# Optimization experiments

Measured on AMD Instinct MI355X. Metric: run time of the kernel, lower is better.

## Reference

```python
import jax, jax.numpy as jnp
import numpy as np

B, T, N, D = 2048, 24, 231, 512
EPS = 1e-5


def _conv(x, W, b):
    # NCHW conv, stride 2, VALID padding (Conv2d k=3, s=2, p=0)
    y = jax.lax.conv_general_dilated(x, W, (2, 2), 'VALID',
                                     dimension_numbers=('NCHW', 'OIHW', 'NCHW'))
    return y + b[None, :, None, None]


def _bn(x, g, b, m, v):
    # inference-mode BatchNorm2d
    inv = jax.lax.rsqrt(v + EPS)
    return (x - m[None, :, None, None]) * (inv * g)[None, :, None, None] + b[None, :, None, None]


def _proj(x, W1, b1, g1, be1, m1, v1, W2, b2, g2, be2, m2, v2):
    y = _bn(jax.nn.relu(_conv(x, W1, b1)), g1, be1, m1, v1)   # [B,32,5,10]
    y = _bn(jax.nn.relu(_conv(y, W2, b2)), g2, be2, m2, v2)   # [B,16,2,4]
    return y


def setup_inputs() -> dict:
    key = jax.random.key(0)
    ks = jax.random.split(key, 16)

    def rn(k, shape, s=1.0):
        return jax.random.normal(k, shape, jnp.float32) * s

    inp = {
        'data0': rn(ks[0], (B, T, N, 2)),
        'data2': rn(ks[1], (B, T, N, 2)),
        'cache': rn(ks[2], (B, 4, 4, N, 4)),
        'timesnet_cache': rn(ks[3], (B, 4, 4, D)),
        'bike_start': rn(ks[4], (B, 4, N)),
        'bike_end': rn(ks[5], (B, 4, N)),
        'taxi_start': rn(ks[6], (B, 4, N)),
        'taxi_end': rn(ks[7], (B, 4, N)),
        'intermediate_output': rn(ks[8], (B, T, D)),
    }
    # conv + batchnorm params for query_proj ('q') and key_proj ('k')
    for pre, i in (('q', 9), ('k', 12)):
        inp[pre + 'W1'] = rn(ks[i], (32, 16, 3, 3), 0.08)
        inp[pre + 'b1'] = jnp.zeros((32,), jnp.float32)
        inp[pre + 'g1'] = jnp.ones((32,), jnp.float32)
        inp[pre + 'be1'] = jnp.zeros((32,), jnp.float32)
        inp[pre + 'm1'] = jnp.zeros((32,), jnp.float32)
        inp[pre + 'v1'] = jnp.ones((32,), jnp.float32)
        inp[pre + 'W2'] = rn(ks[i + 1], (16, 32, 3, 3), 0.06)
        inp[pre + 'b2'] = jnp.zeros((16,), jnp.float32)
        inp[pre + 'g2'] = jnp.ones((16,), jnp.float32)
        inp[pre + 'be2'] = jnp.zeros((16,), jnp.float32)
        inp[pre + 'm2'] = jnp.zeros((16,), jnp.float32)
        inp[pre + 'v2'] = jnp.ones((16,), jnp.float32)
    return inp


def reference(data0, data2, cache, timesnet_cache,
              bike_start, bike_end, taxi_start, taxi_end, intermediate_output,
              qW1, qb1, qg1, qbe1, qm1, qv1, qW2, qb2, qg2, qbe2, qm2, qv2,
              kW1, kb1, kg1, kbe1, km1, kv1, kW2, kb2, kg2, kbe2, km2, kv2):
    # --- cache plumbing (pred_model outputs supplied directly) ---
    new_predict = jnp.stack([bike_start, bike_end, taxi_start, taxi_end], axis=-1)  # [B,4,N,4]
    updated_cache = jnp.concatenate([new_predict[:, None], cache[:, -3:]], axis=1)  # [B,4,4,N,4]
    results = updated_cache[:, :, 0]                                                # [B,4,N,4]
    new_timesnet_cache = jnp.concatenate(
        [intermediate_output[:, -4:, :][:, None], timesnet_cache[:, -3:]], axis=1)  # [B,4,4,D]

    # --- build q, k: [B,16,231] ---
    q = jnp.concatenate([data0[:, -4:], data2[:, -4:]], axis=-1)     # [B,4,N,4]
    q = q.transpose(0, 1, 3, 2).reshape(B, 16, N)
    k = results.transpose(0, 1, 3, 2).reshape(B, 16, N)

    # --- MultiTensorAttention ---
    Q = _proj(q.reshape(B, 16, 11, 21), qW1, qb1, qg1, qbe1, qm1, qv1,
              qW2, qb2, qg2, qbe2, qm2, qv2).reshape(B, 16, -1)       # [B,16,8]
    K = _proj(k.reshape(B, 16, 11, 21), kW1, kb1, kg1, kbe1, km1, kv1,
              kW2, kb2, kg2, kbe2, km2, kv2).reshape(B, 16, -1)       # [B,16,8]
    d_k = Q.shape[-1]
    scores = jnp.einsum('bid,bjd->bij', Q, K) / jnp.sqrt(jnp.float32(d_k))  # [B,16,16]

    # extract the 4 diagonal 4x4 blocks (equivalent to unfold/unfold + stack)
    s = scores.reshape(B, 4, 4, 4, 4)                # [B, blk_i, in_i, blk_j, in_j]
    idx = jnp.arange(4)
    diag = jnp.moveaxis(s[:, idx, :, idx, :], 0, 1)  # [B,4,4,4]
    attn = jax.nn.softmax(diag, axis=-1)
    weights = jnp.mean(attn, axis=2)                 # [B,4,4]

    return (weights, updated_cache, new_predict, new_timesnet_cache)
```

## Files before the change

### kernel.cpp

```cpp
#include <hip/hip_runtime.h>
#include <math.h>


struct ProjParams {
  const float *W1, *b1, *g1, *be1, *m1, *v1;
  const float *W2, *b2, *g2, *be2, *m2, *v2;
};

__global__ __launch_bounds__(256) void proj_kernel(
    const float* __restrict__ data0, const float* __restrict__ data2,
    const float* __restrict__ cache,
    const float* __restrict__ bike_start, const float* __restrict__ bike_end,
    const float* __restrict__ taxi_start, const float* __restrict__ taxi_end,
    ProjParams qp, ProjParams kp,
    float* __restrict__ qbuf, float* __restrict__ kbuf)
{
  const int b   = blockIdx.y;
  const int p   = blockIdx.x;
  const int tid = threadIdx.x;

  __shared__ float xs[16 * 231];
  __shared__ float w1s[144 * 32];
  __shared__ float w2s[288 * 16];
  __shared__ float y1s[32 * 50];
  __shared__ float sc1[32], sh1[32], sc2[16], sh2[16];

  const ProjParams P = p ? kp : qp;

  if (p == 0) {
    for (int e = tid; e < 16 * 231; e += 256) {
      int ic = e / 231, n = e - ic * 231;
      int t = ic >> 2, f = ic & 3;
      const float* src = (f < 2) ? data0 : data2;
      xs[e] = src[((b * 24 + 20 + t) * 231 + n) * 2 + (f & 1)];
    }
  } else {
    for (int e = tid; e < 16 * 231; e += 256) {
      int ic = e / 231, n = e - ic * 231;
      int s = ic >> 2, f = ic & 3;
      float v;
      if (s == 0) {
        const float* src = (f == 0) ? bike_start : (f == 1) ? bike_end
                         : (f == 2) ? taxi_start : taxi_end;
        v = src[b * 924 + n];
      } else {
        v = cache[((b * 4 + s) * 924 + n) * 4 + f];
      }
      xs[e] = v;
    }
  }
  for (int e = tid; e < 4608; e += 256) {
    int oc = e / 144, rem = e - oc * 144;
    w1s[rem * 32 + oc] = P.W1[e];
  }
  for (int e = tid; e < 4608; e += 256) {
    int oc = e / 288, rem = e - oc * 288;
    w2s[rem * 16 + oc] = P.W2[e];
  }
  if (tid < 32) {
    float s = rsqrtf(P.v1[tid] + 1e-5f) * P.g1[tid];
    sc1[tid] = s;
    sh1[tid] = P.be1[tid] - P.m1[tid] * s;
  } else if (tid < 48) {
    int oc = tid - 32;
    float s = rsqrtf(P.v2[oc] + 1e-5f) * P.g2[oc];
    sc2[oc] = s;
    sh2[oc] = P.be2[oc] - P.m2[oc] * s;
  }
  __syncthreads();

  if (tid < 80) {
    const int ocg = tid / 10, r = tid - ocg * 10;
    const int oh = r >> 1, owg = r & 1;
    const int oc0 = ocg * 4, ow0 = owg * 5;
    float acc[4][5];
#pragma unroll
    for (int i = 0; i < 4; ++i) {
      float bi = P.b1[oc0 + i];
#pragma unroll
      for (int j = 0; j < 5; ++j) acc[i][j] = bi;
    }
    for (int ic = 0; ic < 16; ++ic) {
      const float* xrow = &xs[ic * 231 + 2 * oh * 21 + 2 * ow0];
      const float* wrow = &w1s[ic * 9 * 32 + oc0];
#pragma unroll
      for (int kh = 0; kh < 3; ++kh) {
#pragma unroll
        for (int kw = 0; kw < 3; ++kw) {
          const float4 wv = *(const float4*)&wrow[(kh * 3 + kw) * 32];
          const float* xr = &xrow[kh * 21 + kw];
#pragma unroll
          for (int j = 0; j < 5; ++j) {
            float xv = xr[2 * j];
            acc[0][j] += wv.x * xv;
            acc[1][j] += wv.y * xv;
            acc[2][j] += wv.z * xv;
            acc[3][j] += wv.w * xv;
          }
        }
      }
    }
#pragma unroll
    for (int i = 0; i < 4; ++i) {
      float s = sc1[oc0 + i], h = sh1[oc0 + i];
#pragma unroll
      for (int j = 0; j < 5; ++j) {
        float v = fmaxf(acc[i][j], 0.0f);
        y1s[(oc0 + i) * 50 + oh * 10 + ow0 + j] = v * s + h;
      }
    }
  }
  __syncthreads();

  if (tid < 32) {
    const int ocg = tid >> 2, r = tid & 3;
    const int oh = r >> 1, owg = r & 1;
    const int oc0 = ocg * 2, ow0 = owg * 2;
    float acc[2][2];
#pragma unroll
    for (int i = 0; i < 2; ++i) {
      float bi = P.b2[oc0 + i];
      acc[i][0] = bi; acc[i][1] = bi;
    }
    for (int ic = 0; ic < 32; ++ic) {
      const float* yrow = &y1s[ic * 50 + 2 * oh * 10 + 2 * ow0];
      const float* wrow = &w2s[ic * 9 * 16 + oc0];
#pragma unroll
      for (int kh = 0; kh < 3; ++kh) {
#pragma unroll
        for (int kw = 0; kw < 3; ++kw) {
          const float2 wv = *(const float2*)&wrow[(kh * 3 + kw) * 16];
          const float* yr = &yrow[kh * 10 + kw];
#pragma unroll
          for (int j = 0; j < 2; ++j) {
            float yv = yr[2 * j];
            acc[0][j] += wv.x * yv;
            acc[1][j] += wv.y * yv;
          }
        }
      }
    }
    float* outp = p ? kbuf : qbuf;
#pragma unroll
    for (int i = 0; i < 2; ++i) {
      float s = sc2[oc0 + i], h = sh2[oc0 + i];
#pragma unroll
      for (int j = 0; j < 2; ++j) {
        float v = fmaxf(acc[i][j], 0.0f);
        outp[(b * 16 + oc0 + i) * 8 + oh * 4 + ow0 + j] = v * s + h;
      }
    }
  }
}

__global__ __launch_bounds__(256) void copy_kernel(
    const float4* __restrict__ cache4,
    const float* __restrict__ bike_start, const float* __restrict__ bike_end,
    const float* __restrict__ taxi_start, const float* __restrict__ taxi_end,
    const float4* __restrict__ io4, const float4* __restrict__ tc4,
    float4* __restrict__ out4)
{
  const int b   = blockIdx.y;
  const int x   = blockIdx.x;
  const int tid = threadIdx.x;
  float4* out_uc = out4 + 8192;
  float4* out_np = out4 + 7577600;
  float4* out_tc = out4 + 9469952;

  if (x < 11) {
    int i = x * 256 + tid;
    if (i < 2772) {
      out_uc[b * 3696 + 924 + i] = cache4[b * 3696 + 924 + i];
    }
  } else if (x < 15) {
    int e = (x - 11) * 256 + tid;
    if (e < 924) {
      int idx = b * 924 + e;
      float4 v;
      v.x = bike_start[idx];
      v.y = bike_end[idx];
      v.z = taxi_start[idx];
      v.w = taxi_end[idx];
      out_np[idx] = v;
      out_uc[b * 3696 + e] = v;
    }
  } else {
    int r = (x - 15) * 256 + tid;
    int s = r >> 9;
    float4 v;
    if (s == 0) {
      int t = (r >> 7) & 3;
      v = io4[(b * 24 + 20 + t) * 128 + (r & 127)];
    } else {
      v = tc4[b * 2048 + r];
    }
    out_tc[b * 2048 + r] = v;
  }
}

__global__ __launch_bounds__(256) void score_kernel(
    const float* __restrict__ Qb, const float* __restrict__ Kb,
    float* __restrict__ wout)
{
  const int tid = threadIdx.x;
  const int b = blockIdx.x * 4 + (tid >> 6);
  const int l = tid & 63;
  const int a = (l >> 4) & 3, c = (l >> 2) & 3, e = l & 3;
  const float* qrow = Qb + (b * 16 + a * 4 + c) * 8;
  const float* krow = Kb + (b * 16 + a * 4 + e) * 8;
  float dot = 0.0f;
#pragma unroll
  for (int d = 0; d < 8; ++d) dot += qrow[d] * krow[d];
  float v = dot * 0.35355339059327373f;

  float m = fmaxf(v, __shfl_xor(v, 1));
  m = fmaxf(m, __shfl_xor(m, 2));
  float pe = expf(v - m);
  float ssum = pe + __shfl_xor(pe, 1);
  ssum += __shfl_xor(ssum, 2);
  float attn = pe / ssum;

  float t = attn + __shfl_xor(attn, 4);
  t += __shfl_xor(t, 8);
  if (c == 0) wout[b * 16 + a * 4 + e] = 0.25f * t;
}

extern "C" void kernel_launch(void* const* d_in, const int* in_sizes, int n_in,
                              void* d_out, int out_size, void* d_ws, size_t ws_size,
                              hipStream_t stream) {
  const float* data0      = (const float*)d_in[0];
  const float* data2      = (const float*)d_in[1];
  const float* cache      = (const float*)d_in[2];
  const float* tcache     = (const float*)d_in[3];
  const float* bike_start = (const float*)d_in[4];
  const float* bike_end   = (const float*)d_in[5];
  const float* taxi_start = (const float*)d_in[6];
  const float* taxi_end   = (const float*)d_in[7];
  const float* iout       = (const float*)d_in[8];

  ProjParams qp = {
    (const float*)d_in[9],  (const float*)d_in[10], (const float*)d_in[11],
    (const float*)d_in[12], (const float*)d_in[13], (const float*)d_in[14],
    (const float*)d_in[15], (const float*)d_in[16], (const float*)d_in[17],
    (const float*)d_in[18], (const float*)d_in[19], (const float*)d_in[20]
  };
  ProjParams kp = {
    (const float*)d_in[21], (const float*)d_in[22], (const float*)d_in[23],
    (const float*)d_in[24], (const float*)d_in[25], (const float*)d_in[26],
    (const float*)d_in[27], (const float*)d_in[28], (const float*)d_in[29],
    (const float*)d_in[30], (const float*)d_in[31], (const float*)d_in[32]
  };

  float* qbuf = (float*)d_ws;
  float* kbuf = qbuf + 2048 * 16 * 8;
  float* out  = (float*)d_out;

  hipLaunchKernelGGL(proj_kernel, dim3(2, 2048), dim3(256), 0, stream,
                     data0, data2, cache, bike_start, bike_end, taxi_start,
                     taxi_end, qp, kp, qbuf, kbuf);
  hipLaunchKernelGGL(copy_kernel, dim3(23, 2048), dim3(256), 0, stream,
                     (const float4*)cache, bike_start, bike_end, taxi_start,
                     taxi_end, (const float4*)iout, (const float4*)tcache,
                     (float4*)out);
  hipLaunchKernelGGL(score_kernel, dim3(512), dim3(256), 0, stream,
                     qbuf, kbuf, out);
}
```

Before: 721.3 us.

## Pretranspose conv weights once in a prep kernel and vectorize input gathers

Adds a tiny prep kernel that transposes both conv weight sets and folds the BatchNorm scale and shift into a workspace buffer once per call. The per-batch projection blocks then copy W1 into shared memory with float4 loads, read W2 and the BN constants straight from global memory (relying on cache), and drop the w2s shared buffer. Input gathers now use float2 and float4 loads where the source layout allows. The aim is to remove the redundant per-block weight transpose and scattered scalar loads. The cost is an extra launch and uncached-in-LDS global reads of W2 in the second conv.

New measurement: 643.9 us. 10.7% less time.

```diff
diff --git a/kernel.cpp b/kernel.cpp
--- a/kernel.cpp
+++ b/kernel.cpp
@@ -1,11 +1,41 @@
 #include <hip/hip_runtime.h>
 #include <math.h>
 
+
+#define WPATH 9312
 
 struct ProjParams {
   const float *W1, *b1, *g1, *be1, *m1, *v1;
   const float *W2, *b2, *g2, *be2, *m2, *v2;
 };
+
+__global__ __launch_bounds__(256) void prep_kernel(
+    ProjParams qp, ProjParams kp, float* __restrict__ wout)
+{
+  const int p   = blockIdx.x;
+  const int tid = threadIdx.x;
+  const ProjParams P = p ? kp : qp;
+  float* wp = wout + p * WPATH;
+
+  for (int dst = tid; dst < 4608; dst += 256) {
+    int rem = dst >> 5, oc = dst & 31;
+    wp[dst] = P.W1[oc * 144 + rem];
+  }
+  for (int dst = tid; dst < 4608; dst += 256) {
+    int rem = dst >> 4, oc = dst & 15;
+    wp[4608 + dst] = P.W2[oc * 288 + rem];
+  }
+  if (tid < 32) {
+    float s = rsqrtf(P.v1[tid] + 1e-5f) * P.g1[tid];
+    wp[9216 + tid] = s;
+    wp[9248 + tid] = P.be1[tid] - P.m1[tid] * s;
+  } else if (tid < 48) {
+    int oc = tid - 32;
+    float s = rsqrtf(P.v2[oc] + 1e-5f) * P.g2[oc];
+    wp[9280 + oc] = s;
+    wp[9296 + oc] = P.be2[oc] - P.m2[oc] * s;
+  }
+}
 
 __global__ __launch_bounds__(256) void proj_kernel(
     const float* __restrict__ data0, const float* __restrict__ data2,
@@ -13,6 +43,7 @@
     const float* __restrict__ bike_start, const float* __restrict__ bike_end,
     const float* __restrict__ taxi_start, const float* __restrict__ taxi_end,
     ProjParams qp, ProjParams kp,
+    const float* __restrict__ wt,
     float* __restrict__ qbuf, float* __restrict__ kbuf)
 {
   const int b   = blockIdx.y;
@@ -21,51 +52,43 @@
 
   __shared__ float xs[16 * 231];
   __shared__ float w1s[144 * 32];
-  __shared__ float w2s[288 * 16];
   __shared__ float y1s[32 * 50];
-  __shared__ float sc1[32], sh1[32], sc2[16], sh2[16];
 
   const ProjParams P = p ? kp : qp;
+  const float* wp = wt + p * WPATH;
+
+  {
+    const float4* wsrc4 = (const float4*)wp;
+    float4* w1s4 = (float4*)w1s;
+    for (int dst = tid; dst < 1152; dst += 256) w1s4[dst] = wsrc4[dst];
+  }
 
   if (p == 0) {
-    for (int e = tid; e < 16 * 231; e += 256) {
-      int ic = e / 231, n = e - ic * 231;
-      int t = ic >> 2, f = ic & 3;
-      const float* src = (f < 2) ? data0 : data2;
-      xs[e] = src[((b * 24 + 20 + t) * 231 + n) * 2 + (f & 1)];
+    for (int e = tid; e < 1848; e += 256) {
+      int pr = e / 231, n = e - pr * 231;
+      int t = pr >> 1, half = pr & 1;
+      const float2* src = (const float2*)(half ? data2 : data0);
+      float2 v = src[(b * 24 + 20 + t) * 231 + n];
+      int ic0 = t * 4 + half * 2;
+      xs[ic0 * 231 + n]       = v.x;
+      xs[(ic0 + 1) * 231 + n] = v.y;
     }
   } else {
-    for (int e = tid; e < 16 * 231; e += 256) {
-      int ic = e / 231, n = e - ic * 231;
-      int s = ic >> 2, f = ic & 3;
-      float v;
-      if (s == 0) {
-        const float* src = (f == 0) ? bike_start : (f == 1) ? bike_end
-                         : (f == 2) ? taxi_start : taxi_end;
-        v = src[b * 924 + n];
-      } else {
-        v = cache[((b * 4 + s) * 924 + n) * 4 + f];
-      }
-      xs[e] = v;
-    }
-  }
-  for (int e = tid; e < 4608; e += 256) {
-    int oc = e / 144, rem = e - oc * 144;
-    w1s[rem * 32 + oc] = P.W1[e];
-  }
-  for (int e = tid; e < 4608; e += 256) {
-    int oc = e / 288, rem = e - oc * 288;
-    w2s[rem * 16 + oc] = P.W2[e];
-  }
-  if (tid < 32) {
-    float s = rsqrtf(P.v1[tid] + 1e-5f) * P.g1[tid];
-    sc1[tid] = s;
-    sh1[tid] = P.be1[tid] - P.m1[tid] * s;
-  } else if (tid < 48) {
-    int oc = tid - 32;
-    float s = rsqrtf(P.v2[oc] + 1e-5f) * P.g2[oc];
-    sc2[oc] = s;
-    sh2[oc] = P.be2[oc] - P.m2[oc] * s;
+    for (int e = tid; e < 924; e += 256) {
+      int f = e / 231;
+      const float* src = (f == 0) ? bike_start : (f == 1) ? bike_end
+                       : (f == 2) ? taxi_start : taxi_end;
+      xs[e] = src[b * 924 + (e - f * 231)];
+    }
+    for (int e = tid; e < 693; e += 256) {
+      int s = e / 231 + 1, n = e - (s - 1) * 231;
+      float4 v = ((const float4*)cache)[(b * 4 + s) * 924 + n];
+      int ic0 = s * 4;
+      xs[(ic0 + 0) * 231 + n] = v.x;
+      xs[(ic0 + 1) * 231 + n] = v.y;
+      xs[(ic0 + 2) * 231 + n] = v.z;
+      xs[(ic0 + 3) * 231 + n] = v.w;
+    }
   }
   __syncthreads();
 
@@ -100,6 +123,8 @@
         }
       }
     }
+    const float* sc1 = wp + 9216;
+    const float* sh1 = wp + 9248;
 #pragma unroll
     for (int i = 0; i < 4; ++i) {
       float s = sc1[oc0 + i], h = sh1[oc0 + i];
@@ -116,6 +141,7 @@
     const int ocg = tid >> 2, r = tid & 3;
     const int oh = r >> 1, owg = r & 1;
     const int oc0 = ocg * 2, ow0 = owg * 2;
+    const float* w2t = wp + 4608;
     float acc[2][2];
 #pragma unroll
     for (int i = 0; i < 2; ++i) {
@@ -124,7 +150,7 @@
     }
     for (int ic = 0; ic < 32; ++ic) {
       const float* yrow = &y1s[ic * 50 + 2 * oh * 10 + 2 * ow0];
-      const float* wrow = &w2s[ic * 9 * 16 + oc0];
+      const float* wrow = &w2t[ic * 9 * 16 + oc0];
 #pragma unroll
       for (int kh = 0; kh < 3; ++kh) {
 #pragma unroll
@@ -140,6 +166,8 @@
         }
       }
     }
+    const float* sc2 = wp + 9280;
+    const float* sh2 = wp + 9296;
     float* outp = p ? kbuf : qbuf;
 #pragma unroll
     for (int i = 0; i < 2; ++i) {
@@ -251,13 +279,15 @@
     (const float*)d_in[30], (const float*)d_in[31], (const float*)d_in[32]
   };
 
-  float* qbuf = (float*)d_ws;
+  float* wt   = (float*)d_ws;
+  float* qbuf = wt + 2 * WPATH;
   float* kbuf = qbuf + 2048 * 16 * 8;
   float* out  = (float*)d_out;
 
+  hipLaunchKernelGGL(prep_kernel, dim3(2), dim3(256), 0, stream, qp, kp, wt);
   hipLaunchKernelGGL(proj_kernel, dim3(2, 2048), dim3(256), 0, stream,
                      data0, data2, cache, bike_start, bike_end, taxi_start,
-                     taxi_end, qp, kp, qbuf, kbuf);
+                     taxi_end, qp, kp, wt, qbuf, kbuf);
   hipLaunchKernelGGL(copy_kernel, dim3(23, 2048), dim3(256), 0, stream,
                      (const float4*)cache, bike_start, bike_end, taxi_start,
                      taxi_end, (const float4*)iout, (const float4*)tcache,
```
